# Optimization experiments

Measured on AMD Instinct MI355X. Metric: run time of the kernel, lower is better.

## Reference

```python
import jax, jax.numpy as jnp
import numpy as np

N = 2048        # nodes
IN_DIM = 128    # input feature dim
K = 8           # channels
D = 32          # per-channel dim (C_dim)
ITERS = 4       # routing iterations
BETA = 1.0      # attention temperature
EPS = 1e-12     # F.normalize eps


def l2norm(x):
    # F.normalize(x, dim=-1): x / max(||x||_2, eps)
    n = jnp.linalg.norm(x, axis=-1, keepdims=True)
    return x / jnp.maximum(n, EPS)


def setup_inputs() -> dict:
    key = jax.random.key(0)
    k1, k2, k3, k4 = jax.random.split(key, 4)
    adj = jax.random.randint(k1, (N, N), 0, 2, dtype=jnp.int32)
    features = jax.random.normal(k2, (N, IN_DIM), dtype=jnp.float32)
    # parameters initialized ~ N(0,1) as in init_parameters
    W = jax.random.normal(k3, (K, IN_DIM, D), dtype=jnp.float32)
    b = jax.random.normal(k4, (K, D), dtype=jnp.float32)
    return {"adj": adj, "features": features, "W": W, "b": b}


def reference(adj, features, W, b):
    mask = (adj > 0)[None, :, :]                         # [1, N, N]
    # per-channel projection + row L2 normalize -> Z: [K, N, D]
    Z = l2norm(jnp.einsum('nd,kdc->knc', features, W) + b[:, None, :])
    for _ in range(ITERS):
        # per-channel masked attention scores [K, N, N]
        att = jnp.einsum('knc,kmc->knm', Z, Z)
        att = jnp.where(mask, att, 0.0) / BETA
        # softmax across channels (dim=2 in torch after cat == K axis here)
        att = jax.nn.softmax(att, axis=0)
        att = jnp.where(mask, att, 0.0)
        # weighted aggregate + residual + L2 normalize
        Z = l2norm(Z + jnp.einsum('knm,kmc->knc', att, Z))
    # concat channels along feature dim -> [N, K*D]
    return jnp.transpose(Z, (1, 0, 2)).reshape(N, K * D)
```

## Files before the change

### kernel.cpp

```cpp
#include <hip/hip_runtime.h>
#include <hip/hip_bf16.h>
#include <hip/hip_fp16.h>

#define NN 2048
#define KK 8
#define DD 32
#define ZSZ (KK * NN * DD)
#define PSTR 36

#define TW(row, slot) (((row) << 4) + ((((slot) ^ (((row) >> 1) & 3))) << 2))

typedef __attribute__((ext_vector_type(8))) short short8;
typedef __attribute__((ext_vector_type(4))) float f32x4;
typedef __attribute__((ext_vector_type(4))) unsigned int u32x4;

union UU { u32x4 q; short8 v; unsigned int u[4]; };

#define SELHI 0x07060302u
#define SELLO 0x05040100u

__device__ __forceinline__ unsigned int prm(unsigned int a, unsigned int b, unsigned int sel) {
  return __builtin_amdgcn_perm(a, b, sel);
}
__device__ __forceinline__ unsigned int bfr(float x) {
  unsigned int u = __float_as_uint(x);
  return (u + 0x7fffu + ((u >> 16) & 1u)) >> 16;
}
__device__ __forceinline__ float bf2f(unsigned int h) {
  return __uint_as_float(h << 16);
}
__device__ __forceinline__ unsigned int packp(float a, float b) {
  union { __hip_bfloat162 h; unsigned int u; } cv;
  cv.h = __float22bfloat162_rn(make_float2(a, b));
  return cv.u;
}
__device__ __forceinline__ f32x4 MF(short8 a, short8 b, f32x4 c) {
  return __builtin_amdgcn_mfma_f32_16x16x32_bf16(a, b, c, 0, 0, 0);
}
__device__ __forceinline__ short8 as_s8(u32x4 x) { UU u; u.q = x; return u.v; }

__global__ __launch_bounds__(256) void pm_kernel(const float* __restrict__ feat,
                                                 const float* __restrict__ W,
                                                 const float* __restrict__ bias,
                                                 unsigned short* __restrict__ Zghi,
                                                 unsigned short* __restrict__ Zthi,
                                                 const int* __restrict__ adj,
                                                 unsigned int* __restrict__ mbits) {
  const int t = threadIdx.x;
  if (blockIdx.x < 256) {
    const int nb = blockIdx.x * 8;
    const int k = t >> 5, c = t & 31;
    float s[8];
#pragma unroll
    for (int j = 0; j < 8; ++j) s[j] = bias[k * DD + c];
    const float* w = W + (k * 128) * DD + c;
    const float* fp = feat + nb * 128;
#pragma unroll 4
    for (int d = 0; d < 128; ++d) {
      float wv = w[d * DD];
#pragma unroll
      for (int j = 0; j < 8; ++j) s[j] = fmaf(fp[j * 128 + d], wv, s[j]);
    }
    unsigned int hi[8];
#pragma unroll
    for (int j = 0; j < 8; ++j) {
      float sq = s[j] * s[j];
#pragma unroll
      for (int off = 16; off > 0; off >>= 1) sq += __shfl_xor(sq, off, 32);
      float z = s[j] / fmaxf(sqrtf(sq), 1e-12f);
      hi[j] = bfr(z);
      Zghi[(k * NN + nb + j) * DD + c] = (unsigned short)hi[j];
    }
    uint4 tp = make_uint4(hi[0] | (hi[1] << 16), hi[2] | (hi[3] << 16),
                          hi[4] | (hi[5] << 16), hi[6] | (hi[7] << 16));
    *(uint4*)&Zthi[(size_t)k * DD * NN + (size_t)c * NN + nb] = tp;
  } else {
    const int base = (blockIdx.x - 256) * 1024 + t;
    const int lane = t & 63;
    int v[4];
#pragma unroll
    for (int rr = 0; rr < 4; ++rr) v[rr] = adj[base + 256 * rr];
#pragma unroll
    for (int rr = 0; rr < 4; ++rr) {
      int idx = base + 256 * rr;
      unsigned long long b = __ballot(v[rr] > 0);
      if (lane == 0) mbits[idx >> 5] = (unsigned int)b;
      if (lane == 32) mbits[idx >> 5] = (unsigned int)(b >> 32);
    }
  }
}

template <int NCt>
__global__ __launch_bounds__(256) void rp_kernel(const __half* __restrict__ part,
                                                 unsigned short* __restrict__ Zghi,
                                                 unsigned short* __restrict__ Zthi) {
  __shared__ unsigned short T[DD][33];
  const int t = threadIdx.x;
  const int k = blockIdx.x >> 6, mt = blockIdx.x & 63;
  const int m0 = mt * 32;
  const int mloc = t >> 3, c4 = t & 7;
  const size_t idx = (size_t)(k * NN + m0 + mloc) * DD + 4 * c4;
  uint2 zb = *(const uint2*)&Zghi[idx];
  float4 v;
  v.x = bf2f(zb.x & 0xffffu);
  v.y = __uint_as_float(zb.x & 0xffff0000u);
  v.z = bf2f(zb.y & 0xffffu);
  v.w = __uint_as_float(zb.y & 0xffff0000u);
#pragma unroll
  for (int j = 0; j < NCt; ++j) {
    const __half2* ph = (const __half2*)&part[(size_t)j * ZSZ + idx];
    float2 a = __half22float2(ph[0]);
    float2 b = __half22float2(ph[1]);
    v.x += a.x; v.y += a.y; v.z += b.x; v.w += b.y;
  }
  float sq = v.x * v.x + v.y * v.y + v.z * v.z + v.w * v.w;
  sq += __shfl_xor(sq, 1, 8);
  sq += __shfl_xor(sq, 2, 8);
  sq += __shfl_xor(sq, 4, 8);
  const float sc = 1.0f / fmaxf(sqrtf(sq), 1e-12f);
  float z[4] = {v.x * sc, v.y * sc, v.z * sc, v.w * sc};
  unsigned int hi[4];
#pragma unroll
  for (int e = 0; e < 4; ++e) {
    hi[e] = bfr(z[e]);
    T[4 * c4 + e][mloc] = (unsigned short)hi[e];
  }
  *(uint2*)&Zghi[idx] = make_uint2(hi[0] | (hi[1] << 16), hi[2] | (hi[3] << 16));
  __syncthreads();
  const int cloc = t >> 3, m4 = t & 7;
  unsigned int o0 = (unsigned int)T[cloc][4 * m4 + 0] | ((unsigned int)T[cloc][4 * m4 + 1] << 16);
  unsigned int o1 = (unsigned int)T[cloc][4 * m4 + 2] | ((unsigned int)T[cloc][4 * m4 + 3] << 16);
  *(uint2*)&Zthi[(size_t)k * DD * NN + (size_t)cloc * NN + m0 + 4 * m4] = make_uint2(o0, o1);
}

template <int NS>
__global__ __launch_bounds__(256, 2) void iter_kernel(const unsigned short* __restrict__ Zghi,
                                                      const unsigned short* __restrict__ Zthi,
                                                      const unsigned int* __restrict__ mbits,
                                                      __half* __restrict__ part) {
  __shared__ __align__(16) unsigned int lds[8192 + 4 * 4 * 16 * PSTR];
  const int t = threadIdx.x;
  const int w = t >> 6;
  const int lane = t & 63;
  const int l15 = lane & 15;
  const int g = lane >> 4;
  const int nw = blockIdx.x * 64 + w * 16;
  const int mchunk = blockIdx.y * (NS * 32);

  const unsigned int* Zg = (const unsigned int*)Zghi;
  const unsigned int* Zt = (const unsigned int*)Zthi;

  short8 A[KK];
#pragma unroll
  for (int k = 0; k < KK; ++k)
    A[k] = as_s8(*(const u32x4*)&Zg[(size_t)(k * NN + nw + l15) * 16 + 4 * g]);

  unsigned int mwa[4][NS];
#pragma unroll
  for (int r = 0; r < 4; ++r)
#pragma unroll
    for (int q4 = 0; q4 < NS / 4; ++q4) {
      uint4 m4 = *(const uint4*)&mbits[(size_t)(nw + 4 * g + r) * 64 + (mchunk >> 5) + 4 * q4];
      mwa[r][4 * q4 + 0] = m4.x; mwa[r][4 * q4 + 1] = m4.y;
      mwa[r][4 * q4 + 2] = m4.z; mwa[r][4 * q4 + 3] = m4.w;
    }

  f32x4 O[KK][2];
#pragma unroll
  for (int k = 0; k < KK; ++k)
#pragma unroll
    for (int ch = 0; ch < 2; ++ch) O[k][ch] = {0.0f, 0.0f, 0.0f, 0.0f};

  const int sqd = t & 3;
  const int sr0 = t >> 2;

  u32x4 Lgh[4], Lth[4];
  auto do_loads = [&](int mb) {
#pragma unroll
    for (int j = 0; j < 4; ++j) {
      int r = 64 * j + sr0;
      int k = r >> 5, rm = r & 31;
      Lgh[j] = *(const u32x4*)&Zg[(size_t)k * (NN * 16) + (size_t)(mb + rm) * 16 + sqd * 4];
      Lth[j] = *(const u32x4*)&Zt[(size_t)k * (NN * 16) + (size_t)rm * (NN / 2) + (mb >> 1) + sqd * 4];
    }
  };
  do_loads(mchunk);

  unsigned int* Pw = &lds[8192 + w * (4 * 16 * PSTR)];

#pragma unroll
  for (int st = 0; st < NS; ++st) {
    const int mb = mchunk + st * 32;
    __syncthreads();
#pragma unroll
    for (int j = 0; j < 4; ++j) {
      int r = 64 * j + sr0;
      *(u32x4*)&lds[TW(r, sqd)] = Lgh[j];
      *(u32x4*)&lds[4096 + TW(r, sqd)] = Lth[j];
    }
    __syncthreads();
    if (st + 1 < NS) do_loads(mb + 32);

#pragma unroll
    for (int sub = 0; sub < 2; ++sub) {
      f32x4 S[KK];
#pragma unroll
      for (int k = 0; k < KK; ++k) {
        int row = k * 32 + 16 * sub + l15;
        u32x4 bh = *(const u32x4*)&lds[TW(row, g)];
        f32x4 z = {0.0f, 0.0f, 0.0f, 0.0f};
        S[k] = MF(A[k], as_s8(bh), z);
      }
#pragma unroll
      for (int r = 0; r < 4; ++r) {
        float e[KK];
        float sum = 0.0f;
#pragma unroll
        for (int k = 0; k < KK; ++k) { e[k] = __expf(S[k][r]); sum += e[k]; }
        int ml = 16 * sub + l15;
        float f = ((mwa[r][st] >> ml) & 1u) ? __builtin_amdgcn_rcpf(sum) : 0.0f;
#pragma unroll
        for (int k = 0; k < KK; ++k) S[k][r] = e[k] * f;
      }
#pragma unroll
      for (int kp = 0; kp < 4; ++kp)
#pragma unroll
        for (int r = 0; r < 4; ++r) {
          int n = 4 * g + r;
          Pw[kp * (16 * PSTR) + n * PSTR + 16 * sub + l15] =
              packp(S[2 * kp][r], S[2 * kp + 1][r]);
        }
    }

#pragma unroll
    for (int kp = 0; kp < 4; ++kp) {
      const unsigned int* Pr = &Pw[kp * (16 * PSTR) + l15 * PSTR + 8 * g];
      u32x4 a0 = *(const u32x4*)Pr;
      u32x4 a1 = *(const u32x4*)(Pr + 4);
      UU pk0, pk1;
      pk0.u[0] = prm(a0.y, a0.x, SELLO); pk0.u[1] = prm(a0.w, a0.z, SELLO);
      pk0.u[2] = prm(a1.y, a1.x, SELLO); pk0.u[3] = prm(a1.w, a1.z, SELLO);
      pk1.u[0] = prm(a0.y, a0.x, SELHI); pk1.u[1] = prm(a0.w, a0.z, SELHI);
      pk1.u[2] = prm(a1.y, a1.x, SELHI); pk1.u[3] = prm(a1.w, a1.z, SELHI);
#pragma unroll
      for (int kk = 0; kk < 2; ++kk) {
        int k = 2 * kp + kk;
#pragma unroll
        for (int ch = 0; ch < 2; ++ch) {
          int row = k * 32 + 16 * ch + l15;
          u32x4 b = *(const u32x4*)&lds[4096 + TW(row, g)];
          O[k][ch] = MF(kk ? pk1.v : pk0.v, as_s8(b), O[k][ch]);
        }
      }
    }
  }

  __half* dst = part + (size_t)blockIdx.y * ZSZ;
#pragma unroll
  for (int k = 0; k < KK; ++k)
#pragma unroll
    for (int ch = 0; ch < 2; ++ch) {
      f32x4 o = O[k][ch];
#pragma unroll
      for (int r = 0; r < 4; ++r)
        dst[(size_t)(k * NN + nw + 4 * g + r) * DD + 16 * ch + l15] = __float2half_rn(o[r]);
    }
}

template <int NCt>
__global__ __launch_bounds__(256) void ro_kernel(const unsigned short* __restrict__ Zghi,
                                                 const __half* __restrict__ part,
                                                 float* __restrict__ out) {
  const int n = blockIdx.x, t = threadIdx.x;
  const int k = t >> 5, c = t & 31;
  const size_t idx = (size_t)(k * NN + n) * DD + c;
  float v = bf2f((unsigned int)Zghi[idx]);
#pragma unroll
  for (int j = 0; j < NCt; ++j) v += __half2float(part[(size_t)j * ZSZ + idx]);
  float sq = v * v;
#pragma unroll
  for (int off = 16; off > 0; off >>= 1) sq += __shfl_xor(sq, off, 32);
  out[n * (KK * DD) + t] = v / fmaxf(sqrtf(sq), 1e-12f);
}

extern "C" void kernel_launch(void* const* d_in, const int* in_sizes, int n_in,
                              void* d_out, int out_size, void* d_ws, size_t ws_size,
                              hipStream_t stream) {
  const int* adj = (const int*)d_in[0];
  const float* feat = (const float*)d_in[1];
  const float* W = (const float*)d_in[2];
  const float* b = (const float*)d_in[3];
  float* out = (float*)d_out;

  int NC = 16;
  while (NC > 4) {
    size_t need = (size_t)ZSZ * 2 * 2 + (size_t)NN * 64 * 4 + (size_t)NC * ZSZ * 2;
    if (need <= ws_size) break;
    NC >>= 1;
  }

  unsigned short* Zghi = (unsigned short*)d_ws;
  unsigned short* Zthi = Zghi + ZSZ;
  unsigned int* mbits = (unsigned int*)(Zthi + ZSZ);
  __half* part = (__half*)(mbits + NN * 64);

  pm_kernel<<<256 + 4096, 256, 0, stream>>>(feat, W, b, Zghi, Zthi, adj, mbits);

  for (int it = 0; it < 4; ++it) {
    if (NC == 16)
      iter_kernel<4><<<dim3(32, 16), 256, 0, stream>>>(Zghi, Zthi, mbits, part);
    else if (NC == 8)
      iter_kernel<8><<<dim3(32, 8), 256, 0, stream>>>(Zghi, Zthi, mbits, part);
    else
      iter_kernel<16><<<dim3(32, 4), 256, 0, stream>>>(Zghi, Zthi, mbits, part);
    if (it < 3) {
      if (NC == 16)
        rp_kernel<16><<<512, 256, 0, stream>>>(part, Zghi, Zthi);
      else if (NC == 8)
        rp_kernel<8><<<512, 256, 0, stream>>>(part, Zghi, Zthi);
      else
        rp_kernel<4><<<512, 256, 0, stream>>>(part, Zghi, Zthi);
    } else {
      if (NC == 16)
        ro_kernel<16><<<NN, 256, 0, stream>>>(Zghi, part, out);
      else if (NC == 8)
        ro_kernel<8><<<NN, 256, 0, stream>>>(Zghi, part, out);
      else
        ro_kernel<4><<<NN, 256, 0, stream>>>(Zghi, part, out);
    }
  }
}
```

Baseline: 189.1 us.

## Stage features in LDS, issue all score MFMAs up front, set wave priorities

In the projection kernel, the 8-node feature tile is first staged into shared memory, so the inner FMA loop reads LDS instead of repeated global loads. In the attention kernel, the preloaded per-thread mask word array is replaced by a per-stage load of four mask words, which lowers register pressure. The two sub-tile score MFMA batches are now issued back to back before the softmax, and s_setprio raises wave priority around the MFMA sections so matrix work from different waves can overlap with softmax VALU work. The trade-off is a mask load on every stage and more live score registers (S0 and S1 together).

```diff
diff --git a/kernel.cpp b/kernel.cpp
--- a/kernel.cpp
+++ b/kernel.cpp
@@ -46,20 +46,22 @@
                                                  unsigned short* __restrict__ Zthi,
                                                  const int* __restrict__ adj,
                                                  unsigned int* __restrict__ mbits) {
+  __shared__ float fsh[1024];
   const int t = threadIdx.x;
   if (blockIdx.x < 256) {
     const int nb = blockIdx.x * 8;
     const int k = t >> 5, c = t & 31;
+    *(float4*)&fsh[4 * t] = *(const float4*)&feat[nb * 128 + 4 * t];
     float s[8];
 #pragma unroll
     for (int j = 0; j < 8; ++j) s[j] = bias[k * DD + c];
     const float* w = W + (k * 128) * DD + c;
-    const float* fp = feat + nb * 128;
+    __syncthreads();
 #pragma unroll 4
     for (int d = 0; d < 128; ++d) {
       float wv = w[d * DD];
 #pragma unroll
-      for (int j = 0; j < 8; ++j) s[j] = fmaf(fp[j * 128 + d], wv, s[j]);
+      for (int j = 0; j < 8; ++j) s[j] = fmaf(fsh[j * 128 + d], wv, s[j]);
     }
     unsigned int hi[8];
 #pragma unroll
@@ -155,16 +157,6 @@
   for (int k = 0; k < KK; ++k)
     A[k] = as_s8(*(const u32x4*)&Zg[(size_t)(k * NN + nw + l15) * 16 + 4 * g]);
 
-  unsigned int mwa[4][NS];
-#pragma unroll
-  for (int r = 0; r < 4; ++r)
-#pragma unroll
-    for (int q4 = 0; q4 < NS / 4; ++q4) {
-      uint4 m4 = *(const uint4*)&mbits[(size_t)(nw + 4 * g + r) * 64 + (mchunk >> 5) + 4 * q4];
-      mwa[r][4 * q4 + 0] = m4.x; mwa[r][4 * q4 + 1] = m4.y;
-      mwa[r][4 * q4 + 2] = m4.z; mwa[r][4 * q4 + 3] = m4.w;
-    }
-
   f32x4 O[KK][2];
 #pragma unroll
   for (int k = 0; k < KK; ++k)
@@ -188,6 +180,28 @@
 
   unsigned int* Pw = &lds[8192 + w * (4 * 16 * PSTR)];
 
+  auto softmax_store = [&](f32x4* S, int sub, const unsigned int* mw) {
+#pragma unroll
+    for (int r = 0; r < 4; ++r) {
+      float e[KK];
+      float sum = 0.0f;
+#pragma unroll
+      for (int k = 0; k < KK; ++k) { e[k] = __expf(S[k][r]); sum += e[k]; }
+      int ml = 16 * sub + l15;
+      float f = ((mw[r] >> ml) & 1u) ? __builtin_amdgcn_rcpf(sum) : 0.0f;
+#pragma unroll
+      for (int k = 0; k < KK; ++k) S[k][r] = e[k] * f;
+    }
+#pragma unroll
+    for (int kp = 0; kp < 4; ++kp)
+#pragma unroll
+      for (int r = 0; r < 4; ++r) {
+        int n = 4 * g + r;
+        Pw[kp * (16 * PSTR) + n * PSTR + 16 * sub + l15] =
+            packp(S[2 * kp][r], S[2 * kp + 1][r]);
+      }
+  };
+
 #pragma unroll
   for (int st = 0; st < NS; ++st) {
     const int mb = mchunk + st * 32;
@@ -201,37 +215,31 @@
     __syncthreads();
     if (st + 1 < NS) do_loads(mb + 32);
 
-#pragma unroll
-    for (int sub = 0; sub < 2; ++sub) {
-      f32x4 S[KK];
-#pragma unroll
-      for (int k = 0; k < KK; ++k) {
-        int row = k * 32 + 16 * sub + l15;
-        u32x4 bh = *(const u32x4*)&lds[TW(row, g)];
-        f32x4 z = {0.0f, 0.0f, 0.0f, 0.0f};
-        S[k] = MF(A[k], as_s8(bh), z);
-      }
-#pragma unroll
-      for (int r = 0; r < 4; ++r) {
-        float e[KK];
-        float sum = 0.0f;
-#pragma unroll
-        for (int k = 0; k < KK; ++k) { e[k] = __expf(S[k][r]); sum += e[k]; }
-        int ml = 16 * sub + l15;
-        float f = ((mwa[r][st] >> ml) & 1u) ? __builtin_amdgcn_rcpf(sum) : 0.0f;
-#pragma unroll
-        for (int k = 0; k < KK; ++k) S[k][r] = e[k] * f;
-      }
-#pragma unroll
-      for (int kp = 0; kp < 4; ++kp)
-#pragma unroll
-        for (int r = 0; r < 4; ++r) {
-          int n = 4 * g + r;
-          Pw[kp * (16 * PSTR) + n * PSTR + 16 * sub + l15] =
-              packp(S[2 * kp][r], S[2 * kp + 1][r]);
-        }
-    }
-
+    unsigned int mw[4];
+#pragma unroll
+    for (int r = 0; r < 4; ++r)
+      mw[r] = mbits[(size_t)(nw + 4 * g + r) * 64 + (mb >> 5)];
+
+    f32x4 S0[KK], S1[KK];
+    __builtin_amdgcn_s_setprio(1);
+#pragma unroll
+    for (int k = 0; k < KK; ++k) {
+      u32x4 bh = *(const u32x4*)&lds[TW(k * 32 + l15, g)];
+      f32x4 z = {0.0f, 0.0f, 0.0f, 0.0f};
+      S0[k] = MF(A[k], as_s8(bh), z);
+    }
+#pragma unroll
+    for (int k = 0; k < KK; ++k) {
+      u32x4 bh = *(const u32x4*)&lds[TW(k * 32 + 16 + l15, g)];
+      f32x4 z = {0.0f, 0.0f, 0.0f, 0.0f};
+      S1[k] = MF(A[k], as_s8(bh), z);
+    }
+    __builtin_amdgcn_s_setprio(0);
+
+    softmax_store(S0, 0, mw);
+    softmax_store(S1, 1, mw);
+
+    __builtin_amdgcn_s_setprio(1);
 #pragma unroll
     for (int kp = 0; kp < 4; ++kp) {
       const unsigned int* Pr = &Pw[kp * (16 * PSTR) + l15 * PSTR + 8 * g];
@@ -253,6 +261,7 @@
         }
       }
     }
+    __builtin_amdgcn_s_setprio(0);
   }
 
   __half* dst = part + (size_t)blockIdx.y * ZSZ;
```

New measurement: 190.0 us. Within noise of the previous version (+0.5%).

## Transpose score MFMA to feed softmax output directly into 16x16x16 MFMAs

Applied to the files above, without the earlier changes.

Swaps the MFMA operand order for the score product so each lane's score accumulators already form the A-operand layout of a 16x16x16 bf16 MFMA. This removes the LDS round trip and permute shuffle that previously re-laid-out the probabilities before the aggregation MFMA. The score-tile staging also moves to a double-buffered LDS scheme with one barrier per step, and the mask bits are loaded as one word per lane. Separately, the projection kernel stages its feature rows in shared memory. In exchange the aggregation uses twice as many smaller MFMAs, and the LDS footprint changes, which may affect occupancy.

```diff
diff --git a/kernel.cpp b/kernel.cpp
--- a/kernel.cpp
+++ b/kernel.cpp
@@ -6,22 +6,18 @@
 #define KK 8
 #define DD 32
 #define ZSZ (KK * NN * DD)
-#define PSTR 36
 
 #define TW(row, slot) (((row) << 4) + ((((slot) ^ (((row) >> 1) & 3))) << 2))
+#define TW2(row, wo) (((row) << 4) + (((((wo) >> 2) ^ (((row) >> 1) & 3))) << 2) + ((wo) & 3))
 
 typedef __attribute__((ext_vector_type(8))) short short8;
+typedef __attribute__((ext_vector_type(4))) short short4v;
 typedef __attribute__((ext_vector_type(4))) float f32x4;
 typedef __attribute__((ext_vector_type(4))) unsigned int u32x4;
 
 union UU { u32x4 q; short8 v; unsigned int u[4]; };
-
-#define SELHI 0x07060302u
-#define SELLO 0x05040100u
-
-__device__ __forceinline__ unsigned int prm(unsigned int a, unsigned int b, unsigned int sel) {
-  return __builtin_amdgcn_perm(a, b, sel);
-}
+union U2 { uint2 q; short4v v; unsigned int u[2]; };
+
 __device__ __forceinline__ unsigned int bfr(float x) {
   unsigned int u = __float_as_uint(x);
   return (u + 0x7fffu + ((u >> 16) & 1u)) >> 16;
@@ -36,6 +32,9 @@
 }
 __device__ __forceinline__ f32x4 MF(short8 a, short8 b, f32x4 c) {
   return __builtin_amdgcn_mfma_f32_16x16x32_bf16(a, b, c, 0, 0, 0);
+}
+__device__ __forceinline__ f32x4 MF16(short4v a, short4v b, f32x4 c) {
+  return __builtin_amdgcn_mfma_f32_16x16x16bf16_1k(a, b, c, 0, 0, 0);
 }
 __device__ __forceinline__ short8 as_s8(u32x4 x) { UU u; u.q = x; return u.v; }
 
@@ -46,20 +45,22 @@
                                                  unsigned short* __restrict__ Zthi,
                                                  const int* __restrict__ adj,
                                                  unsigned int* __restrict__ mbits) {
+  __shared__ float fsh[1024];
   const int t = threadIdx.x;
   if (blockIdx.x < 256) {
     const int nb = blockIdx.x * 8;
     const int k = t >> 5, c = t & 31;
+    *(float4*)&fsh[4 * t] = *(const float4*)&feat[nb * 128 + 4 * t];
     float s[8];
 #pragma unroll
     for (int j = 0; j < 8; ++j) s[j] = bias[k * DD + c];
     const float* w = W + (k * 128) * DD + c;
-    const float* fp = feat + nb * 128;
+    __syncthreads();
 #pragma unroll 4
     for (int d = 0; d < 128; ++d) {
       float wv = w[d * DD];
 #pragma unroll
-      for (int j = 0; j < 8; ++j) s[j] = fmaf(fp[j * 128 + d], wv, s[j]);
+      for (int j = 0; j < 8; ++j) s[j] = fmaf(fsh[j * 128 + d], wv, s[j]);
     }
     unsigned int hi[8];
 #pragma unroll
@@ -138,7 +139,7 @@
                                                       const unsigned short* __restrict__ Zthi,
                                                       const unsigned int* __restrict__ mbits,
                                                       __half* __restrict__ part) {
-  __shared__ __align__(16) unsigned int lds[8192 + 4 * 4 * 16 * PSTR];
+  __shared__ __align__(16) unsigned int lds[2][8192];
   const int t = threadIdx.x;
   const int w = t >> 6;
   const int lane = t & 63;
@@ -155,15 +156,13 @@
   for (int k = 0; k < KK; ++k)
     A[k] = as_s8(*(const u32x4*)&Zg[(size_t)(k * NN + nw + l15) * 16 + 4 * g]);
 
-  unsigned int mwa[4][NS];
-#pragma unroll
-  for (int r = 0; r < 4; ++r)
-#pragma unroll
-    for (int q4 = 0; q4 < NS / 4; ++q4) {
-      uint4 m4 = *(const uint4*)&mbits[(size_t)(nw + 4 * g + r) * 64 + (mchunk >> 5) + 4 * q4];
-      mwa[r][4 * q4 + 0] = m4.x; mwa[r][4 * q4 + 1] = m4.y;
-      mwa[r][4 * q4 + 2] = m4.z; mwa[r][4 * q4 + 3] = m4.w;
-    }
+  unsigned int mword[NS];
+#pragma unroll
+  for (int q4 = 0; q4 < NS / 4; ++q4) {
+    uint4 m4 = *(const uint4*)&mbits[(size_t)(nw + l15) * 64 + (mchunk >> 5) + 4 * q4];
+    mword[4 * q4 + 0] = m4.x; mword[4 * q4 + 1] = m4.y;
+    mword[4 * q4 + 2] = m4.z; mword[4 * q4 + 3] = m4.w;
+  }
 
   f32x4 O[KK][2];
 #pragma unroll
@@ -184,32 +183,35 @@
       Lth[j] = *(const u32x4*)&Zt[(size_t)k * (NN * 16) + (size_t)rm * (NN / 2) + (mb >> 1) + sqd * 4];
     }
   };
-  do_loads(mchunk);
-
-  unsigned int* Pw = &lds[8192 + w * (4 * 16 * PSTR)];
-
-#pragma unroll
-  for (int st = 0; st < NS; ++st) {
-    const int mb = mchunk + st * 32;
-    __syncthreads();
+  auto wr = [&](int buf) {
 #pragma unroll
     for (int j = 0; j < 4; ++j) {
       int r = 64 * j + sr0;
-      *(u32x4*)&lds[TW(r, sqd)] = Lgh[j];
-      *(u32x4*)&lds[4096 + TW(r, sqd)] = Lth[j];
-    }
-    __syncthreads();
-    if (st + 1 < NS) do_loads(mb + 32);
-
+      *(u32x4*)&lds[buf][TW(r, sqd)] = Lgh[j];
+      *(u32x4*)&lds[buf][4096 + TW(r, sqd)] = Lth[j];
+    }
+  };
+
+  do_loads(mchunk);
+  wr(0);
+  if (NS > 1) do_loads(mchunk + 32);
+  __syncthreads();
+
+#pragma unroll
+  for (int st = 0; st < NS; ++st) {
+    const unsigned int* B = lds[st & 1];
+    if (st + 1 < NS) wr((st + 1) & 1);
+    if (st + 2 < NS) do_loads(mchunk + (st + 2) * 32);
+
+    const unsigned int mw = mword[st];
 #pragma unroll
     for (int sub = 0; sub < 2; ++sub) {
       f32x4 S[KK];
 #pragma unroll
       for (int k = 0; k < KK; ++k) {
-        int row = k * 32 + 16 * sub + l15;
-        u32x4 bh = *(const u32x4*)&lds[TW(row, g)];
+        u32x4 bh = *(const u32x4*)&B[TW(k * 32 + 16 * sub + l15, g)];
         f32x4 z = {0.0f, 0.0f, 0.0f, 0.0f};
-        S[k] = MF(A[k], as_s8(bh), z);
+        S[k] = MF(as_s8(bh), A[k], z);
       }
 #pragma unroll
       for (int r = 0; r < 4; ++r) {
@@ -217,42 +219,25 @@
         float sum = 0.0f;
 #pragma unroll
         for (int k = 0; k < KK; ++k) { e[k] = __expf(S[k][r]); sum += e[k]; }
-        int ml = 16 * sub + l15;
-        float f = ((mwa[r][st] >> ml) & 1u) ? __builtin_amdgcn_rcpf(sum) : 0.0f;
+        float f = ((mw >> (16 * sub + 4 * g + r)) & 1u) ? __builtin_amdgcn_rcpf(sum) : 0.0f;
 #pragma unroll
         for (int k = 0; k < KK; ++k) S[k][r] = e[k] * f;
       }
 #pragma unroll
-      for (int kp = 0; kp < 4; ++kp)
-#pragma unroll
-        for (int r = 0; r < 4; ++r) {
-          int n = 4 * g + r;
-          Pw[kp * (16 * PSTR) + n * PSTR + 16 * sub + l15] =
-              packp(S[2 * kp][r], S[2 * kp + 1][r]);
-        }
-    }
-
-#pragma unroll
-    for (int kp = 0; kp < 4; ++kp) {
-      const unsigned int* Pr = &Pw[kp * (16 * PSTR) + l15 * PSTR + 8 * g];
-      u32x4 a0 = *(const u32x4*)Pr;
-      u32x4 a1 = *(const u32x4*)(Pr + 4);
-      UU pk0, pk1;
-      pk0.u[0] = prm(a0.y, a0.x, SELLO); pk0.u[1] = prm(a0.w, a0.z, SELLO);
-      pk0.u[2] = prm(a1.y, a1.x, SELLO); pk0.u[3] = prm(a1.w, a1.z, SELLO);
-      pk1.u[0] = prm(a0.y, a0.x, SELHI); pk1.u[1] = prm(a0.w, a0.z, SELHI);
-      pk1.u[2] = prm(a1.y, a1.x, SELHI); pk1.u[3] = prm(a1.w, a1.z, SELHI);
-#pragma unroll
-      for (int kk = 0; kk < 2; ++kk) {
-        int k = 2 * kp + kk;
+      for (int k = 0; k < KK; ++k) {
+        U2 pa;
+        pa.u[0] = packp(S[k][0], S[k][1]);
+        pa.u[1] = packp(S[k][2], S[k][3]);
 #pragma unroll
         for (int ch = 0; ch < 2; ++ch) {
           int row = k * 32 + 16 * ch + l15;
-          u32x4 b = *(const u32x4*)&lds[4096 + TW(row, g)];
-          O[k][ch] = MF(kk ? pk1.v : pk0.v, as_s8(b), O[k][ch]);
+          U2 bv;
+          bv.q = *(const uint2*)&B[4096 + TW2(row, 8 * sub + 2 * g)];
+          O[k][ch] = MF16(pa.v, bv.v, O[k][ch]);
         }
       }
     }
+    __syncthreads();
   }
 
   __half* dst = part + (size_t)blockIdx.y * ZSZ;
```

Result: faster. 182.0 us (-3.7%).
